# Kernel optimization log

Hardware: AMD Instinct MI355X
Metric: run time of the kernel (lower is better)

The kernel has to match this reference:

```python
import jax, jax.numpy as jnp
import numpy as np

NEG_INF = -1e30  # used via float('-inf') in original; -inf literal is fine too


def setup_inputs() -> dict:
    key = jax.random.key(0)
    kq, kk, kv = jax.random.split(key, 3)
    b, h, s, d = 2, 32, 2048, 128
    q = jax.random.normal(kq, (b, h, s, d), dtype=jnp.float32)
    k = jax.random.normal(kk, (b, h, s, d), dtype=jnp.float32)
    v = jax.random.normal(kv, (b, h, s, d), dtype=jnp.float32)
    # causal mask, True = masked (matches the module's `~tril` path when mask is None)
    mask = ~jnp.tril(jnp.ones((s, s), dtype=bool))
    attention_mask = jnp.broadcast_to(mask[None, None], (b, 1, s, s))
    return {"query_layer": q, "key_layer": k, "value_layer": v,
            "attention_mask": attention_mask}


def reference(query_layer, key_layer, value_layer, attention_mask):
    b, h, sq, hd = query_layer.shape
    norm_factor = jnp.sqrt(jnp.asarray(hd, dtype=query_layer.dtype))
    # scores: [b, h, sq, sk], computed in fp32 as in the original (.float())
    scores = jnp.einsum('bhqd,bhkd->bhqk', query_layer, key_layer) / norm_factor
    scores = scores.astype(jnp.float32)
    scores = jnp.where(attention_mask, -jnp.inf, scores)
    probs = jax.nn.softmax(scores, axis=-1).astype(value_layer.dtype)
    # context: [b, h, sq, hd]
    ctx = jnp.einsum('bhqk,bhkd->bhqd', probs, value_layer)
    # -> [b, sq, h*hd]
    ctx = jnp.transpose(ctx, (0, 2, 1, 3)).reshape(b, sq, h * hd)
    return ctx
```

## Files before the change

kernel.cpp:

```cpp
#include <hip/hip_runtime.h>
#include <hip/hip_bf16.h>

typedef __attribute__((ext_vector_type(8))) short bf16x8;
typedef __attribute__((ext_vector_type(8))) unsigned short u16x8;
typedef __attribute__((ext_vector_type(4))) float f32x4;

#define S_LEN 2048
#define D_DIM 128
#define BH_NUM 64
#define OUT_W 4096

__device__ __forceinline__ unsigned short f2bf(float f){
  unsigned int u = __float_as_uint(f);
  u += 0x7FFFu + ((u >> 16) & 1u);
  return (unsigned short)(u >> 16);
}

__device__ __forceinline__ short pbf(float f){
  __hip_bfloat16 h = __float2bfloat16(f);
  return *reinterpret_cast<short*>(&h);
}

__device__ __forceinline__ void gl_lds16(const void* g, void* l){
  __builtin_amdgcn_global_load_lds(
      (const __attribute__((address_space(1))) unsigned int*)g,
      (__attribute__((address_space(3))) unsigned int*)l, 16, 0, 0);
}

__global__ __launch_bounds__(256) void conv_bf16(const float* __restrict__ in,
                                                 unsigned short* __restrict__ out, int n8){
  int i = blockIdx.x * 256 + threadIdx.x;
  if (i < n8){
    const float4* p = (const float4*)(in + (size_t)i * 8);
    float4 a = p[0], b = p[1];
    u16x8 o;
    o[0]=f2bf(a.x); o[1]=f2bf(a.y); o[2]=f2bf(a.z); o[3]=f2bf(a.w);
    o[4]=f2bf(b.x); o[5]=f2bf(b.y); o[6]=f2bf(b.z); o[7]=f2bf(b.w);
    *(u16x8*)(out + (size_t)i * 8) = o;
  }
}

__global__ __launch_bounds__(256) void conv_vt(const float* __restrict__ V,
                                               unsigned short* __restrict__ Vt){
  __shared__ unsigned short lt[256][36];
  const int t = threadIdx.x;
  const int key0 = blockIdx.x * 256;
  const int d0   = blockIdx.y * 32;
  const int bh   = blockIdx.z;
  const float* src = V + ((size_t)bh * S_LEN + key0 + t) * D_DIM + d0;
  #pragma unroll
  for (int j = 0; j < 8; ++j){
    float4 v = *(const float4*)(src + j * 4);
    ushort4 pk; pk.x=f2bf(v.x); pk.y=f2bf(v.y); pk.z=f2bf(v.z); pk.w=f2bf(v.w);
    *(ushort4*)&lt[t][j * 4] = pk;
  }
  __syncthreads();
  #pragma unroll
  for (int uu = 0; uu < 4; ++uu){
    int u  = uu * 256 + t;
    int d  = u >> 5;
    int j8 = u & 31;
    int b64 = j8 >> 3, m8 = j8 & 7;
    int ks2 = m8 >> 2, t4m = m8 & 3;
    u16x8 o;
    #pragma unroll
    for (int i = 0; i < 8; ++i){
      int srck = b64 * 64 + ks2 * 32 + (i >> 2) * 16 + t4m * 4 + (i & 3);
      o[i] = lt[srck][d];
    }
    *(u16x8*)(Vt + ((size_t)bh * D_DIM + d0 + d) * S_LEN + key0 + j8 * 8) = o;
  }
}

__device__ __forceinline__ void tile_compute(
    const unsigned short* __restrict__ kb, const unsigned short* __restrict__ vb,
    const bf16x8 (&qf0)[4], const bf16x8 (&qf1)[4],
    f32x4 (&o0)[8], f32x4 (&o1)[8],
    float& m0r, float& l0, float& m1r, float& l1,
    int kvb, int qw0, int qw1, int c, int t4)
{
  const int cx = c & 7;
  const float THR = 11.5f;
  f32x4 s0[2], s1[2];
  #pragma unroll
  for (int g = 0; g < 2; ++g){ s0[g] = (f32x4){0,0,0,0}; s1[g] = (f32x4){0,0,0,0}; }
  __builtin_amdgcn_s_setprio(1);
  #pragma unroll
  for (int g = 0; g < 2; ++g){
    const unsigned short* krow = kb + (size_t)(g * 16 + c) * D_DIM;
    #pragma unroll
    for (int ks = 0; ks < 4; ++ks){
      bf16x8 kf = *(const bf16x8*)(krow + (((ks * 4 + t4) ^ cx) * 8));
      s0[g] = __builtin_amdgcn_mfma_f32_16x16x32_bf16(kf, qf0[ks], s0[g], 0, 0, 0);
      s1[g] = __builtin_amdgcn_mfma_f32_16x16x32_bf16(kf, qf1[ks], s1[g], 0, 0, 0);
    }
  }
  __builtin_amdgcn_s_setprio(0);
  if (kvb + 31 > qw0){
    int q = qw0 + c;
    #pragma unroll
    for (int g = 0; g < 2; ++g)
      #pragma unroll
      for (int r = 0; r < 4; ++r)
        if (kvb + g * 16 + t4 * 4 + r > q) s0[g][r] = -1e30f;
  }
  if (kvb + 31 > qw1){
    int q = qw1 + c;
    #pragma unroll
    for (int g = 0; g < 2; ++g)
      #pragma unroll
      for (int r = 0; r < 4; ++r)
        if (kvb + g * 16 + t4 * 4 + r > q) s1[g][r] = -1e30f;
  }
  float mt0 = fmaxf(fmaxf(fmaxf(s0[0][0], s0[0][1]), fmaxf(s0[0][2], s0[0][3])),
                    fmaxf(fmaxf(s0[1][0], s0[1][1]), fmaxf(s0[1][2], s0[1][3])));
  float mt1 = fmaxf(fmaxf(fmaxf(s1[0][0], s1[0][1]), fmaxf(s1[0][2], s1[0][3])),
                    fmaxf(fmaxf(s1[1][0], s1[1][1]), fmaxf(s1[1][2], s1[1][3])));
  mt0 = fmaxf(mt0, __shfl_xor(mt0, 16));
  mt0 = fmaxf(mt0, __shfl_xor(mt0, 32));
  mt1 = fmaxf(mt1, __shfl_xor(mt1, 16));
  mt1 = fmaxf(mt1, __shfl_xor(mt1, 32));
  float a0 = 1.f, a1 = 1.f;
  float dmax = fmaxf(mt0 - m0r, mt1 - m1r);
  if (!__all(dmax <= THR)){
    float n0 = fmaxf(m0r, mt0), n1 = fmaxf(m1r, mt1);
    a0 = exp2f(m0r - n0); a1 = exp2f(m1r - n1);
    m0r = n0; m1r = n1;
    float b0[4], b1[4];
    #pragma unroll
    for (int r = 0; r < 4; ++r){
      b0[r] = __shfl(a0, t4 * 4 + r);
      b1[r] = __shfl(a1, t4 * 4 + r);
    }
    #pragma unroll
    for (int db = 0; db < 8; ++db)
      #pragma unroll
      for (int r = 0; r < 4; ++r){ o0[db][r] *= b0[r]; o1[db][r] *= b1[r]; }
  }
  float rs0 = 0.f, rs1 = 0.f;
  bf16x8 p0, p1;
  #pragma unroll
  for (int g = 0; g < 2; ++g)
    #pragma unroll
    for (int r = 0; r < 4; ++r){
      float e0 = exp2f(s0[g][r] - m0r); rs0 += e0; p0[g*4+r] = pbf(e0);
      float e1 = exp2f(s1[g][r] - m1r); rs1 += e1; p1[g*4+r] = pbf(e1);
    }
  rs0 += __shfl_xor(rs0, 16); rs0 += __shfl_xor(rs0, 32);
  rs1 += __shfl_xor(rs1, 16); rs1 += __shfl_xor(rs1, 32);
  l0 = l0 * a0 + rs0;
  l1 = l1 * a1 + rs1;
  __builtin_amdgcn_s_setprio(1);
  #pragma unroll
  for (int db = 0; db < 8; ++db){
    const unsigned short* vrow = vb + (size_t)(db * 16 + c) * 32;
    bf16x8 vf = *(const bf16x8*)(vrow + ((t4 ^ (c & 3)) * 8));
    o0[db] = __builtin_amdgcn_mfma_f32_16x16x32_bf16(p0, vf, o0[db], 0, 0, 0);
    o1[db] = __builtin_amdgcn_mfma_f32_16x16x32_bf16(p1, vf, o1[db], 0, 0, 0);
  }
  __builtin_amdgcn_s_setprio(0);
}

__global__ __launch_bounds__(256, 3) void attn_fwd_bf16(
    const float* __restrict__ Qg, const unsigned short* __restrict__ Kw,
    const unsigned short* __restrict__ Vw, float* __restrict__ Og)
{
  __shared__ unsigned short Kl[2][32 * 128];
  __shared__ unsigned short Vl[2][128 * 32];

  const int tid  = threadIdx.x;
  const int lane = tid & 63;
  const int w    = tid >> 6;
  const int c    = lane & 15;
  const int t4   = lane >> 4;
  const int bh   = blockIdx.x;
  const int tq   = 15 - blockIdx.y;
  const unsigned short* Kbh = Kw + (size_t)bh * S_LEN * D_DIM;
  const unsigned short* Vbh = Vw + (size_t)bh * S_LEN * D_DIM;
  const float* Qbh = Qg + (size_t)bh * S_LEN * D_DIM;
  const int bi = bh >> 5, hh = bh & 31;
  const float QS = 0.12751743f;

  const int q0  = tq * 128;
  const int qw0 = q0 + 32 * w;
  const int qw1 = qw0 + 16;

  bf16x8 qf0[4], qf1[4];
  {
    const float* r0 = Qbh + (size_t)(qw0 + c) * D_DIM + t4 * 8;
    const float* r1 = Qbh + (size_t)(qw1 + c) * D_DIM + t4 * 8;
    #pragma unroll
    for (int ks = 0; ks < 4; ++ks){
      float4 a = *(const float4*)(r0 + ks * 32);
      float4 b = *(const float4*)(r0 + ks * 32 + 4);
      bf16x8 f;
      f[0]=pbf(a.x*QS); f[1]=pbf(a.y*QS); f[2]=pbf(a.z*QS); f[3]=pbf(a.w*QS);
      f[4]=pbf(b.x*QS); f[5]=pbf(b.y*QS); f[6]=pbf(b.z*QS); f[7]=pbf(b.w*QS);
      qf0[ks] = f;
      a = *(const float4*)(r1 + ks * 32);
      b = *(const float4*)(r1 + ks * 32 + 4);
      f[0]=pbf(a.x*QS); f[1]=pbf(a.y*QS); f[2]=pbf(a.z*QS); f[3]=pbf(a.w*QS);
      f[4]=pbf(b.x*QS); f[5]=pbf(b.y*QS); f[6]=pbf(b.z*QS); f[7]=pbf(b.w*QS);
      qf1[ks] = f;
    }
  }

  f32x4 o0[8], o1[8];
  #pragma unroll
  for (int db = 0; db < 8; ++db){ o0[db] = (f32x4){0,0,0,0}; o1[db] = (f32x4){0,0,0,0}; }
  float m0r = -1e30f, l0 = 0.f, m1r = -1e30f, l1 = 0.f;

  const int ch1 = tid + 256;
  const unsigned short* ks0 = Kbh + (size_t)(tid >> 4) * D_DIM + (((tid & 15) ^ ((tid >> 4) & 7)) * 8);
  const unsigned short* ks1 = Kbh + (size_t)(ch1 >> 4) * D_DIM + (((ch1 & 15) ^ ((ch1 >> 4) & 7)) * 8);
  const unsigned short* vs0 = Vbh + (size_t)(tid >> 2) * S_LEN + (((tid & 3) ^ ((tid >> 2) & 3)) * 8);
  const unsigned short* vs1 = Vbh + (size_t)(ch1 >> 2) * S_LEN + (((ch1 & 3) ^ ((ch1 >> 2) & 3)) * 8);
  const int du0 = w * 512;
  const int du1 = 2048 + w * 512;

  #define STAGE(KB, VB) do { \
      gl_lds16(ks0, (KB) + du0); gl_lds16(ks1, (KB) + du1); \
      gl_lds16(vs0, (VB) + du0); gl_lds16(vs1, (VB) + du1); \
      ks0 += 32 * D_DIM; ks1 += 32 * D_DIM; vs0 += 32; vs1 += 32; } while(0)

  const int nt   = 4 * tq + 4;
  const int kmax = qw0 + 31;

  STAGE(Kl[0], Vl[0]);
  for (int it = 0; it < nt; it += 2){
    __syncthreads();
    STAGE(Kl[1], Vl[1]);
    if (it * 32 <= kmax)
      tile_compute(Kl[0], Vl[0], qf0, qf1, o0, o1, m0r, l0, m1r, l1,
                   it * 32, qw0, qw1, c, t4);
    __syncthreads();
    if (it + 2 < nt)
      STAGE(Kl[0], Vl[0]);
    if ((it + 1) * 32 <= kmax)
      tile_compute(Kl[1], Vl[1], qf0, qf1, o0, o1, m0r, l0, m1r, l1,
                   (it + 1) * 32, qw0, qw1, c, t4);
  }
  #undef STAGE

  float* ob0 = Og + ((size_t)bi * S_LEN + qw0) * OUT_W + hh * D_DIM;
  float* ob1 = Og + ((size_t)bi * S_LEN + qw1) * OUT_W + hh * D_DIM;
  #pragma unroll
  for (int r = 0; r < 4; ++r){
    float lr0 = __shfl(l0, t4 * 4 + r), lr1 = __shfl(l1, t4 * 4 + r);
    float i0 = 1.0f / lr0, i1 = 1.0f / lr1;
    float* w0 = ob0 + (size_t)(t4 * 4 + r) * OUT_W;
    float* w1 = ob1 + (size_t)(t4 * 4 + r) * OUT_W;
    #pragma unroll
    for (int db = 0; db < 8; ++db){
      w0[db * 16 + c] = o0[db][r] * i0;
      w1[db * 16 + c] = o1[db][r] * i1;
    }
  }
}

__global__ __launch_bounds__(256) void attn_fwd(
    const float* __restrict__ Qg, const float* __restrict__ Kg,
    const float* __restrict__ Vg, float* __restrict__ Og)
{
  __shared__ unsigned short Kfb[32][136];
  __shared__ unsigned short Vfb[128][40];
  const int tid  = threadIdx.x;
  const int lane = tid & 63;
  const int w    = tid >> 6;
  const int c    = lane & 15;
  const int t4   = lane >> 4;
  const int q0 = blockIdx.x * 64;
  const int bh = blockIdx.y;
  const size_t base = (size_t)bh * S_LEN * D_DIM;
  const float* Qp = Qg + base;
  const float* Kp = Kg + base;
  const float* Vp = Vg + base;
  const int qw = q0 + w * 16;
  const float QSCALE = 0.08838834764831845f;
  bf16x8 qf[4];
  {
    const float* qrow = Qp + (size_t)(qw + c) * D_DIM + t4 * 8;
    #pragma unroll
    for (int ks = 0; ks < 4; ++ks){
      float4 a = *(const float4*)(qrow + ks * 32);
      float4 b = *(const float4*)(qrow + ks * 32 + 4);
      bf16x8 f;
      f[0]=(short)f2bf(a.x*QSCALE); f[1]=(short)f2bf(a.y*QSCALE);
      f[2]=(short)f2bf(a.z*QSCALE); f[3]=(short)f2bf(a.w*QSCALE);
      f[4]=(short)f2bf(b.x*QSCALE); f[5]=(short)f2bf(b.y*QSCALE);
      f[6]=(short)f2bf(b.z*QSCALE); f[7]=(short)f2bf(b.w*QSCALE);
      qf[ks] = f;
    }
  }
  f32x4 o[8];
  #pragma unroll
  for (int db = 0; db < 8; ++db) o[db] = (f32x4){0.f,0.f,0.f,0.f};
  float m_run = -1e30f, l_run = 0.f;
  const int ntiles = q0 / 32 + 2;
  for (int it = 0; it < ntiles; ++it){
    const int kvb = it * 32;
    #pragma unroll
    for (int rr = 0; rr < 4; ++rr){
      int f   = rr * 256 + tid;
      int key = f >> 5;
      int d0  = (f & 31) * 4;
      float4 k4 = *(const float4*)(Kp + (size_t)(kvb + key) * D_DIM + d0);
      ushort4 pk;
      pk.x = f2bf(k4.x); pk.y = f2bf(k4.y); pk.z = f2bf(k4.z); pk.w = f2bf(k4.w);
      *(ushort4*)&Kfb[key][d0] = pk;
      float4 v4 = *(const float4*)(Vp + (size_t)(kvb + key) * D_DIM + d0);
      int kp = ((key & 15) >> 2) * 8 + (key >> 4) * 4 + (key & 3);
      Vfb[d0 + 0][kp] = f2bf(v4.x);
      Vfb[d0 + 1][kp] = f2bf(v4.y);
      Vfb[d0 + 2][kp] = f2bf(v4.z);
      Vfb[d0 + 3][kp] = f2bf(v4.w);
    }
    __syncthreads();
    if (kvb <= qw + 15){
      f32x4 sg[2];
      #pragma unroll
      for (int g = 0; g < 2; ++g){
        f32x4 acc = (f32x4){0.f,0.f,0.f,0.f};
        #pragma unroll
        for (int ks = 0; ks < 4; ++ks){
          bf16x8 kf = *(const bf16x8*)&Kfb[g*16 + c][ks*32 + t4*8];
          acc = __builtin_amdgcn_mfma_f32_16x16x32_bf16(kf, qf[ks], acc, 0, 0, 0);
        }
        sg[g] = acc;
      }
      if (kvb + 31 > qw){
        int q = qw + c;
        #pragma unroll
        for (int g = 0; g < 2; ++g)
          #pragma unroll
          for (int r = 0; r < 4; ++r){
            int key = kvb + g*16 + t4*4 + r;
            if (key > q) sg[g][r] = -1e30f;
          }
      }
      float mt = sg[0][0];
      #pragma unroll
      for (int g = 0; g < 2; ++g)
        #pragma unroll
        for (int r = 0; r < 4; ++r) mt = fmaxf(mt, sg[g][r]);
      mt = fmaxf(mt, __shfl_xor(mt, 16));
      mt = fmaxf(mt, __shfl_xor(mt, 32));
      float m_new = fmaxf(m_run, mt);
      float alpha = __expf(m_run - m_new);
      m_run = m_new;
      float p[8];
      float rs = 0.f;
      #pragma unroll
      for (int i = 0; i < 8; ++i){
        p[i] = __expf(sg[i>>2][i&3] - m_new);
        rs += p[i];
      }
      rs += __shfl_xor(rs, 16);
      rs += __shfl_xor(rs, 32);
      l_run = l_run * alpha + rs;
      bf16x8 pf;
      #pragma unroll
      for (int i = 0; i < 8; ++i) pf[i] = (short)f2bf(p[i]);
      float a_out[4];
      #pragma unroll
      for (int r = 0; r < 4; ++r) a_out[r] = __shfl(alpha, t4*4 + r);
      #pragma unroll
      for (int db = 0; db < 8; ++db){
        #pragma unroll
        for (int r = 0; r < 4; ++r) o[db][r] *= a_out[r];
      }
      #pragma unroll
      for (int db = 0; db < 8; ++db){
        bf16x8 vf = *(const bf16x8*)&Vfb[db*16 + c][t4*8];
        o[db] = __builtin_amdgcn_mfma_f32_16x16x32_bf16(pf, vf, o[db], 0, 0, 0);
      }
    }
    __syncthreads();
  }
  const int bi = bh >> 5;
  const int h  = bh & 31;
  float* obase = Og + ((size_t)bi * S_LEN + qw) * OUT_W + h * D_DIM;
  #pragma unroll
  for (int r = 0; r < 4; ++r){
    float lr  = __shfl(l_run, t4*4 + r);
    float inv = 1.0f / lr;
    float* orow = obase + (size_t)(t4*4 + r) * OUT_W;
    #pragma unroll
    for (int db = 0; db < 8; ++db)
      orow[db*16 + c] = o[db][r] * inv;
  }
}

extern "C" void kernel_launch(void* const* d_in, const int* in_sizes, int n_in,
                              void* d_out, int out_size, void* d_ws, size_t ws_size,
                              hipStream_t stream)
{
  const float* Q = (const float*)d_in[0];
  const float* K = (const float*)d_in[1];
  const float* V = (const float*)d_in[2];
  float* O = (float*)d_out;
  const size_t elems = (size_t)BH_NUM * S_LEN * D_DIM;
  const size_t need  = elems * 2 * 2;
  if (ws_size >= need){
    unsigned short* Kw = (unsigned short*)d_ws;
    unsigned short* Vt = Kw + elems;
    conv_bf16<<<(int)(elems / 8 / 256), 256, 0, stream>>>(K, Kw, (int)(elems / 8));
    conv_vt<<<dim3(S_LEN / 256, D_DIM / 32, BH_NUM), 256, 0, stream>>>(V, Vt);
    attn_fwd_bf16<<<dim3(BH_NUM, 16), 256, 0, stream>>>(Q, Kw, Vt, O);
  } else {
    attn_fwd<<<dim3(S_LEN / 64, BH_NUM), 256, 0, stream>>>(Q, K, V, O);
  }
}
```

Baseline: 150.3 us.

## Switch attention kernel to 32x32x16 MFMA tiles with permlane32 softmax reductions

Replaces the 16x16x32 MFMA tiling, where each wave handled two 16-row query groups, with one 32x32x16 MFMA per wave covering 32 query rows. Row max and sum reductions now use permlane32_swap instead of multiple shuffles, and P is packed with v_cvt_pk_bf16_f32 plus lane swaps to form the A operand. The V transpose layout is simplified to match the new fragment ordering. The aim is fewer MFMA issues, fewer cross-lane ops and less conversion overhead, with the risk of register pressure from the 16-wide accumulators and correctness depending on the new fragment and layout mapping.

Measured after the change: 253.5 us. 68.6% more time.

```diff
diff --git a/kernel.cpp b/kernel.cpp
--- a/kernel.cpp
+++ b/kernel.cpp
@@ -1,9 +1,12 @@
 #include <hip/hip_runtime.h>
 #include <hip/hip_bf16.h>
 
-typedef __attribute__((ext_vector_type(8))) short bf16x8;
-typedef __attribute__((ext_vector_type(8))) unsigned short u16x8;
-typedef __attribute__((ext_vector_type(4))) float f32x4;
+typedef __attribute__((ext_vector_type(8)))  short bf16x8;
+typedef __attribute__((ext_vector_type(8)))  unsigned short u16x8;
+typedef __attribute__((ext_vector_type(4)))  float f32x4;
+typedef __attribute__((ext_vector_type(16))) float f32x16;
+typedef __attribute__((ext_vector_type(4)))  int i32x4;
+typedef __attribute__((ext_vector_type(2)))  int i32x2;
 
 #define S_LEN 2048
 #define D_DIM 128
@@ -19,6 +22,25 @@
 __device__ __forceinline__ short pbf(float f){
   __hip_bfloat16 h = __float2bfloat16(f);
   return *reinterpret_cast<short*>(&h);
+}
+
+__device__ __forceinline__ int cvtpk(float lo, float hi){
+  int r;
+  asm("v_cvt_pk_bf16_f32 %0, %1, %2" : "=v"(r) : "v"(lo), "v"(hi));
+  return r;
+}
+
+__device__ __forceinline__ i32x2 pl32swap(int a, int b){
+  return __builtin_amdgcn_permlane32_swap(a, b, false, false);
+}
+
+__device__ __forceinline__ float xhalf_max(float x){
+  i32x2 r = pl32swap(__float_as_int(x), __float_as_int(x));
+  return fmaxf(__int_as_float(r[0]), __int_as_float(r[1]));
+}
+__device__ __forceinline__ float xhalf_add(float x){
+  i32x2 r = pl32swap(__float_as_int(x), __float_as_int(x));
+  return __int_as_float(r[0]) + __int_as_float(r[1]);
 }
 
 __device__ __forceinline__ void gl_lds16(const void* g, void* l){
@@ -60,103 +82,95 @@
     int u  = uu * 256 + t;
     int d  = u >> 5;
     int j8 = u & 31;
-    int b64 = j8 >> 3, m8 = j8 & 7;
-    int ks2 = m8 >> 2, t4m = m8 & 3;
     u16x8 o;
     #pragma unroll
-    for (int i = 0; i < 8; ++i){
-      int srck = b64 * 64 + ks2 * 32 + (i >> 2) * 16 + t4m * 4 + (i & 3);
-      o[i] = lt[srck][d];
-    }
+    for (int i = 0; i < 8; ++i) o[i] = lt[j8 * 8 + i][d];
     *(u16x8*)(Vt + ((size_t)bh * D_DIM + d0 + d) * S_LEN + key0 + j8 * 8) = o;
   }
 }
 
-__device__ __forceinline__ void tile_compute(
+__device__ __forceinline__ void tile32(
     const unsigned short* __restrict__ kb, const unsigned short* __restrict__ vb,
-    const bf16x8 (&qf0)[4], const bf16x8 (&qf1)[4],
-    f32x4 (&o0)[8], f32x4 (&o1)[8],
-    float& m0r, float& l0, float& m1r, float& l1,
-    int kvb, int qw0, int qw1, int c, int t4)
+    const bf16x8 (&qf)[8], f32x16 (&o)[4],
+    float& mr, float& lr, int kvb, int qw, int j, int h)
 {
-  const int cx = c & 7;
   const float THR = 11.5f;
-  f32x4 s0[2], s1[2];
-  #pragma unroll
-  for (int g = 0; g < 2; ++g){ s0[g] = (f32x4){0,0,0,0}; s1[g] = (f32x4){0,0,0,0}; }
+
+  bf16x8 vf0[4], vf1[4];
+  #pragma unroll
+  for (int db = 0; db < 4; ++db){
+    const unsigned short* vrow = vb + (size_t)(db * 32 + j) * 32;
+    vf0[db] = *(const bf16x8*)(vrow + (((0 + h) ^ (j & 3)) * 8));
+    vf1[db] = *(const bf16x8*)(vrow + (((2 + h) ^ (j & 3)) * 8));
+  }
+
+  f32x16 s;
+  #pragma unroll
+  for (int r = 0; r < 16; ++r) s[r] = 0.f;
   __builtin_amdgcn_s_setprio(1);
   #pragma unroll
-  for (int g = 0; g < 2; ++g){
-    const unsigned short* krow = kb + (size_t)(g * 16 + c) * D_DIM;
-    #pragma unroll
-    for (int ks = 0; ks < 4; ++ks){
-      bf16x8 kf = *(const bf16x8*)(krow + (((ks * 4 + t4) ^ cx) * 8));
-      s0[g] = __builtin_amdgcn_mfma_f32_16x16x32_bf16(kf, qf0[ks], s0[g], 0, 0, 0);
-      s1[g] = __builtin_amdgcn_mfma_f32_16x16x32_bf16(kf, qf1[ks], s1[g], 0, 0, 0);
-    }
+  for (int ks = 0; ks < 8; ++ks){
+    bf16x8 kf = *(const bf16x8*)(kb + (size_t)j * D_DIM + (((2 * ks + h) ^ (j & 7)) * 8));
+    s = __builtin_amdgcn_mfma_f32_32x32x16_bf16(kf, qf[ks], s, 0, 0, 0);
   }
   __builtin_amdgcn_s_setprio(0);
-  if (kvb + 31 > qw0){
-    int q = qw0 + c;
-    #pragma unroll
-    for (int g = 0; g < 2; ++g)
-      #pragma unroll
-      for (int r = 0; r < 4; ++r)
-        if (kvb + g * 16 + t4 * 4 + r > q) s0[g][r] = -1e30f;
-  }
-  if (kvb + 31 > qw1){
-    int q = qw1 + c;
-    #pragma unroll
-    for (int g = 0; g < 2; ++g)
-      #pragma unroll
-      for (int r = 0; r < 4; ++r)
-        if (kvb + g * 16 + t4 * 4 + r > q) s1[g][r] = -1e30f;
-  }
-  float mt0 = fmaxf(fmaxf(fmaxf(s0[0][0], s0[0][1]), fmaxf(s0[0][2], s0[0][3])),
-                    fmaxf(fmaxf(s0[1][0], s0[1][1]), fmaxf(s0[1][2], s0[1][3])));
-  float mt1 = fmaxf(fmaxf(fmaxf(s1[0][0], s1[0][1]), fmaxf(s1[0][2], s1[0][3])),
-                    fmaxf(fmaxf(s1[1][0], s1[1][1]), fmaxf(s1[1][2], s1[1][3])));
-  mt0 = fmaxf(mt0, __shfl_xor(mt0, 16));
-  mt0 = fmaxf(mt0, __shfl_xor(mt0, 32));
-  mt1 = fmaxf(mt1, __shfl_xor(mt1, 16));
-  mt1 = fmaxf(mt1, __shfl_xor(mt1, 32));
-  float a0 = 1.f, a1 = 1.f;
-  float dmax = fmaxf(mt0 - m0r, mt1 - m1r);
-  if (!__all(dmax <= THR)){
-    float n0 = fmaxf(m0r, mt0), n1 = fmaxf(m1r, mt1);
-    a0 = exp2f(m0r - n0); a1 = exp2f(m1r - n1);
-    m0r = n0; m1r = n1;
-    float b0[4], b1[4];
-    #pragma unroll
-    for (int r = 0; r < 4; ++r){
-      b0[r] = __shfl(a0, t4 * 4 + r);
-      b1[r] = __shfl(a1, t4 * 4 + r);
-    }
-    #pragma unroll
-    for (int db = 0; db < 8; ++db)
-      #pragma unroll
-      for (int r = 0; r < 4; ++r){ o0[db][r] *= b0[r]; o1[db][r] *= b1[r]; }
-  }
-  float rs0 = 0.f, rs1 = 0.f;
-  bf16x8 p0, p1;
-  #pragma unroll
-  for (int g = 0; g < 2; ++g)
-    #pragma unroll
-    for (int r = 0; r < 4; ++r){
-      float e0 = exp2f(s0[g][r] - m0r); rs0 += e0; p0[g*4+r] = pbf(e0);
-      float e1 = exp2f(s1[g][r] - m1r); rs1 += e1; p1[g*4+r] = pbf(e1);
-    }
-  rs0 += __shfl_xor(rs0, 16); rs0 += __shfl_xor(rs0, 32);
-  rs1 += __shfl_xor(rs1, 16); rs1 += __shfl_xor(rs1, 32);
-  l0 = l0 * a0 + rs0;
-  l1 = l1 * a1 + rs1;
+
+  if (kvb + 31 > qw){
+    int q = qw + j;
+    #pragma unroll
+    for (int r = 0; r < 16; ++r){
+      int key = kvb + (r & 3) + 8 * (r >> 2) + 4 * h;
+      if (key > q) s[r] = -1e30f;
+    }
+  }
+
+  float t0 = fmaxf(fmaxf(s[0], s[1]),  fmaxf(s[2], s[3]));
+  float t1 = fmaxf(fmaxf(s[4], s[5]),  fmaxf(s[6], s[7]));
+  float t2 = fmaxf(fmaxf(s[8], s[9]),  fmaxf(s[10], s[11]));
+  float t3 = fmaxf(fmaxf(s[12], s[13]), fmaxf(s[14], s[15]));
+  float mt = xhalf_max(fmaxf(fmaxf(t0, t1), fmaxf(t2, t3)));
+
+  float a0 = 1.f;
+  if (!__all(mt - mr <= THR)){
+    float n = fmaxf(mr, mt);
+    a0 = exp2f(mr - n);
+    mr = n;
+    #pragma unroll
+    for (int r = 0; r < 16; ++r){
+      float ar = __shfl(a0, (r & 3) + 8 * (r >> 2) + 4 * h);
+      #pragma unroll
+      for (int db = 0; db < 4; ++db) o[db][r] *= ar;
+    }
+  }
+
+  float p[16];
+  #pragma unroll
+  for (int r = 0; r < 16; ++r) p[r] = exp2f(s[r] - mr);
+  float u0 = (p[0] + p[1]) + (p[2] + p[3]);
+  float u1 = (p[4] + p[5]) + (p[6] + p[7]);
+  float u2 = (p[8] + p[9]) + (p[10] + p[11]);
+  float u3 = (p[12] + p[13]) + (p[14] + p[15]);
+  float rs = xhalf_add((u0 + u1) + (u2 + u3));
+  lr = lr * a0 + rs;
+
+  int w0 = cvtpk(p[0],  p[1]),  w1 = cvtpk(p[2],  p[3]);
+  int w2 = cvtpk(p[4],  p[5]),  w3 = cvtpk(p[6],  p[7]);
+  int w4 = cvtpk(p[8],  p[9]),  w5 = cvtpk(p[10], p[11]);
+  int w6 = cvtpk(p[12], p[13]), w7 = cvtpk(p[14], p[15]);
+  i32x2 r02 = pl32swap(w0, w2);
+  i32x2 r13 = pl32swap(w1, w3);
+  i32x2 r46 = pl32swap(w4, w6);
+  i32x2 r57 = pl32swap(w5, w7);
+  i32x4 A0 = {r02[0], r13[0], r02[1], r13[1]};
+  i32x4 A1 = {r46[0], r57[0], r46[1], r57[1]};
+  bf16x8 pa0 = __builtin_bit_cast(bf16x8, A0);
+  bf16x8 pa1 = __builtin_bit_cast(bf16x8, A1);
+
   __builtin_amdgcn_s_setprio(1);
   #pragma unroll
-  for (int db = 0; db < 8; ++db){
-    const unsigned short* vrow = vb + (size_t)(db * 16 + c) * 32;
-    bf16x8 vf = *(const bf16x8*)(vrow + ((t4 ^ (c & 3)) * 8));
-    o0[db] = __builtin_amdgcn_mfma_f32_16x16x32_bf16(p0, vf, o0[db], 0, 0, 0);
-    o1[db] = __builtin_amdgcn_mfma_f32_16x16x32_bf16(p1, vf, o1[db], 0, 0, 0);
+  for (int db = 0; db < 4; ++db){
+    o[db] = __builtin_amdgcn_mfma_f32_32x32x16_bf16(pa0, vf0[db], o[db], 0, 0, 0);
+    o[db] = __builtin_amdgcn_mfma_f32_32x32x16_bf16(pa1, vf1[db], o[db], 0, 0, 0);
   }
   __builtin_amdgcn_s_setprio(0);
 }
@@ -171,8 +185,8 @@
   const int tid  = threadIdx.x;
   const int lane = tid & 63;
   const int w    = tid >> 6;
-  const int c    = lane & 15;
-  const int t4   = lane >> 4;
+  const int j    = lane & 31;
+  const int h    = lane >> 5;
   const int bh   = blockIdx.x;
   const int tq   = 15 - blockIdx.y;
   const unsigned short* Kbh = Kw + (size_t)bh * S_LEN * D_DIM;
@@ -181,34 +195,29 @@
   const int bi = bh >> 5, hh = bh & 31;
   const float QS = 0.12751743f;
 
-  const int q0  = tq * 128;
-  const int qw0 = q0 + 32 * w;
-  const int qw1 = qw0 + 16;
-
-  bf16x8 qf0[4], qf1[4];
+  const int q0 = tq * 128;
+  const int qw = q0 + 32 * w;
+
+  bf16x8 qf[8];
   {
-    const float* r0 = Qbh + (size_t)(qw0 + c) * D_DIM + t4 * 8;
-    const float* r1 = Qbh + (size_t)(qw1 + c) * D_DIM + t4 * 8;
-    #pragma unroll
-    for (int ks = 0; ks < 4; ++ks){
-      float4 a = *(const float4*)(r0 + ks * 32);
-      float4 b = *(const float4*)(r0 + ks * 32 + 4);
+    const float* qrow = Qbh + (size_t)(qw + j) * D_DIM + h * 8;
+    #pragma unroll
+    for (int ks = 0; ks < 8; ++ks){
+      float4 a = *(const float4*)(qrow + ks * 16);
+      float4 b = *(const float4*)(qrow + ks * 16 + 4);
       bf16x8 f;
       f[0]=pbf(a.x*QS); f[1]=pbf(a.y*QS); f[2]=pbf(a.z*QS); f[3]=pbf(a.w*QS);
       f[4]=pbf(b.x*QS); f[5]=pbf(b.y*QS); f[6]=pbf(b.z*QS); f[7]=pbf(b.w*QS);
-      qf0[ks] = f;
-      a = *(const float4*)(r1 + ks * 32);
-      b = *(const float4*)(r1 + ks * 32 + 4);
-      f[0]=pbf(a.x*QS); f[1]=pbf(a.y*QS); f[2]=pbf(a.z*QS); f[3]=pbf(a.w*QS);
-      f[4]=pbf(b.x*QS); f[5]=pbf(b.y*QS); f[6]=pbf(b.z*QS); f[7]=pbf(b.w*QS);
-      qf1[ks] = f;
-    }
-  }
-
-  f32x4 o0[8], o1[8];
-  #pragma unroll
-  for (int db = 0; db < 8; ++db){ o0[db] = (f32x4){0,0,0,0}; o1[db] = (f32x4){0,0,0,0}; }
-  float m0r = -1e30f, l0 = 0.f, m1r = -1e30f, l1 = 0.f;
+      qf[ks] = f;
+    }
+  }
+
+  f32x16 o[4];
+  #pragma unroll
+  for (int db = 0; db < 4; ++db)
+    #pragma unroll
+    for (int r = 0; r < 16; ++r) o[db][r] = 0.f;
+  float mr = -1e30f, lr = 0.f;
 
   const int ch1 = tid + 256;
   const unsigned short* ks0 = Kbh + (size_t)(tid >> 4) * D_DIM + (((tid & 15) ^ ((tid >> 4) & 7)) * 8);
@@ -224,37 +233,32 @@
       ks0 += 32 * D_DIM; ks1 += 32 * D_DIM; vs0 += 32; vs1 += 32; } while(0)
 
   const int nt   = 4 * tq + 4;
-  const int kmax = qw0 + 31;
+  const int kmax = qw + 31;
 
   STAGE(Kl[0], Vl[0]);
   for (int it = 0; it < nt; it += 2){
     __syncthreads();
     STAGE(Kl[1], Vl[1]);
     if (it * 32 <= kmax)
-      tile_compute(Kl[0], Vl[0], qf0, qf1, o0, o1, m0r, l0, m1r, l1,
-                   it * 32, qw0, qw1, c, t4);
+      tile32(Kl[0], Vl[0], qf, o, mr, lr, it * 32, qw, j, h);
     __syncthreads();
     if (it + 2 < nt)
       STAGE(Kl[0], Vl[0]);
     if ((it + 1) * 32 <= kmax)
-      tile_compute(Kl[1], Vl[1], qf0, qf1, o0, o1, m0r, l0, m1r, l1,
-                   (it + 1) * 32, qw0, qw1, c, t4);
+      tile32(Kl[1], Vl[1], qf, o, mr, lr, (it + 1) * 32, qw, j, h);
   }
   #undef STAGE
 
-  float* ob0 = Og + ((size_t)bi * S_LEN + qw0) * OUT_W + hh * D_DIM;
-  float* ob1 = Og + ((size_t)bi * S_LEN + qw1) * OUT_W + hh * D_DIM;
-  #pragma unroll
-  for (int r = 0; r < 4; ++r){
-    float lr0 = __shfl(l0, t4 * 4 + r), lr1 = __shfl(l1, t4 * 4 + r);
-    float i0 = 1.0f / lr0, i1 = 1.0f / lr1;
-    float* w0 = ob0 + (size_t)(t4 * 4 + r) * OUT_W;
-    float* w1 = ob1 + (size_t)(t4 * 4 + r) * OUT_W;
-    #pragma unroll
-    for (int db = 0; db < 8; ++db){
-      w0[db * 16 + c] = o0[db][r] * i0;
-      w1[db * 16 + c] = o1[db][r] * i1;
-    }
+  float inv = 1.0f / lr;
+  float* ob = Og + ((size_t)bi * S_LEN + qw) * OUT_W + hh * D_DIM;
+  #pragma unroll
+  for (int r = 0; r < 16; ++r){
+    int row = (r & 3) + 8 * (r >> 2) + 4 * h;
+    float ir = __shfl(inv, row);
+    float* orow = ob + (size_t)row * OUT_W;
+    #pragma unroll
+    for (int db = 0; db < 4; ++db)
+      orow[db * 32 + j] = o[db][r] * ir;
   }
 }
 
@@ -378,12 +382,12 @@
     __syncthreads();
   }
   const int bi = bh >> 5;
-  const int h  = bh & 31;
-  float* obase = Og + ((size_t)bi * S_LEN + qw) * OUT_W + h * D_DIM;
+  const int hfb = bh & 31;
+  float* obase = Og + ((size_t)bi * S_LEN + qw) * OUT_W + hfb * D_DIM;
   #pragma unroll
   for (int r = 0; r < 4; ++r){
-    float lr  = __shfl(l_run, t4*4 + r);
-    float inv = 1.0f / lr;
+    float lrr = __shfl(l_run, t4*4 + r);
+    float inv = 1.0f / lrr;
     float* orow = obase + (size_t)(t4*4 + r) * OUT_W;
     #pragma unroll
     for (int db = 0; db < 8; ++db)
```
